# Kernel tuning notes

Hardware: AMD Instinct MI355X
Metric: run time of the kernel (lower is better)

The kernel has to match this reference:

```python
import jax, jax.numpy as jnp
import numpy as np

B_SZ, L_SEQ = 8, 2048
D_MODEL, N_STATE = 1024, 64
NUM_HEADS, N_REC = 1, 8
H_DIM = D_MODEL // NUM_HEADS


def setup_inputs() -> dict:
    key = jax.random.key(0)
    ks = jax.random.split(key, 12)
    Np = N_STATE
    return {
        "u": jax.random.normal(ks[0], (B_SZ, L_SEQ, D_MODEL), jnp.float32),
        "k_proj_w": jax.random.normal(ks[1], (D_MODEL, D_MODEL), jnp.float32) / np.float32(np.sqrt(D_MODEL)),
        "k_proj_b": jax.random.normal(ks[2], (D_MODEL,), jnp.float32) * 0.02,
        "shift_B": jax.random.normal(ks[3], (D_MODEL, Np), jnp.float32) / np.float32(np.sqrt(Np)),
        "shift_C": jax.random.normal(ks[4], (D_MODEL, Np), jnp.float32) / np.float32(np.sqrt(Np)),
        "ssm_k_D": jax.random.normal(ks[5], (D_MODEL,), jnp.float32),
        "log_dt": jax.random.uniform(ks[6], (H_DIM,), jnp.float32, minval=np.float32(np.log(1e-3)), maxval=np.float32(np.log(1e-1))),
        "log_A_real": jnp.log(0.5 * jnp.ones((H_DIM, Np), jnp.float32)),
        "A_imag": jnp.broadcast_to(np.float32(np.pi) * jnp.arange(Np, dtype=jnp.float32), (H_DIM, Np)),
        "B_re": jax.random.normal(ks[7], (H_DIM, Np), jnp.float32),
        "B_im": jax.random.normal(ks[8], (H_DIM, Np), jnp.float32),
    }


def _shift_kernel(Bp, Cp, L):
    # Shift-SSM kernel (SSKernel mode='shift'): K(l) = sum_m C[m+l] * B[m], zero for l >= N.
    N = Bp.shape[-1]
    nfft = 2 * N
    Bf = jnp.fft.rfft(Bp, n=nfft)
    Cf = jnp.fft.rfft(Cp, n=nfft)
    k = jnp.fft.irfft(Cf * jnp.conj(Bf), n=nfft)[..., :N]  # (D, N) linear cross-correlation
    return jnp.pad(k, ((0, 0), (0, L - N)))  # (D, L)


def _kernel_expand(k, log_dt, log_A_real, A_imag, B_re, B_im):
    # Diagonal-SSM state expansion: SSM states x_t = sum_{s<=t} dA^{t-s} dB u_s,
    # read out at N_REC evenly spaced chunk boundaries.
    # k: (B, G, H, L) real -> (B, N_REC, G, H, N) real
    Bb, G, H, L = k.shape
    Lc = L // N_REC
    dt = jnp.exp(log_dt)[:, None]                      # (H,1)
    A = -jnp.exp(log_A_real) + 1j * A_imag             # (H,N)
    dA_log = dt * A                                    # (H,N)
    dB = (B_re + 1j * B_im) * ((jnp.exp(dA_log) - 1.0) / A)  # ZOH discretization
    exps = jnp.arange(Lc - 1, -1, -1, dtype=jnp.float32)      # (Lc,)
    P = jnp.exp(dA_log[..., None] * exps) * dB[..., None]     # (H,N,Lc): dA^{Lc-1-i} dB
    kc = k.reshape(Bb, G, H, N_REC, Lc).astype(P.dtype)
    contrib = jnp.einsum('hnl,bghrl->rbghn', P, kc)           # (N_REC,B,G,H,N)
    dA_Lc = jnp.exp(dA_log * Lc)                              # (H,N)
    x0 = jnp.zeros((Bb, G, H, A.shape[-1]), P.dtype)

    def step(x, c):
        x = dA_Lc * x + c
        return x, x

    _, states = jax.lax.scan(step, x0, contrib)               # (N_REC,B,G,H,N)
    return jnp.transpose(states.real, (1, 0, 2, 3, 4))


def reference(u, k_proj_w, k_proj_b, shift_B, shift_C, ssm_k_D, log_dt, log_A_real, A_imag, B_re, B_im):
    Bb, L, D = u.shape
    # k = W @ u^T + b  -> (B, D, L)
    k = jnp.einsum('bld,hd->bhl', u, k_proj_w) + k_proj_b[None, :, None]
    Ks = _shift_kernel(shift_B, shift_C, L)  # (D, L)
    nfft = 2 * L  # fft_size = L_kernel + L
    conv = jnp.fft.irfft(jnp.fft.rfft(Ks, n=nfft)[None] * jnp.fft.rfft(k, n=nfft), n=nfft)[..., :L]
    k = conv + ssm_k_D[None, :, None] * k
    # rearrange 'b (h d1) l -> b d1 h l'
    k = k.reshape(Bb, H_DIM, NUM_HEADS, L).transpose(0, 2, 1, 3)
    return _kernel_expand(k, log_dt, log_A_real, A_imag, B_re, B_im)
```

## Files before the change

kernel.cpp:

```cpp
#include <hip/hip_runtime.h>
#include <cstddef>
#include <cstdint>

#define L_SEQ 2048
#define DM    1024
#define NREC  8
#define BM 128
#define BN 128
#define BK 32
#define NT (DM / BK)

typedef __attribute__((ext_vector_type(8))) short short8;
typedef __attribute__((ext_vector_type(4))) float f32x4;
typedef __attribute__((ext_vector_type(2))) unsigned int u32x2;

__device__ inline unsigned short f2bf(float f) {
    unsigned u = __float_as_uint(f);
    unsigned r = (u + 0x7FFFu + ((u >> 16) & 1u)) >> 16;
    return (unsigned short)r;
}
__device__ inline float bf2f(unsigned short s) {
    return __uint_as_float(((unsigned)s) << 16);
}
__device__ inline void gload_lds16(const void* g, void* l) {
    __builtin_amdgcn_global_load_lds(
        (const __attribute__((address_space(1))) void*)g,
        (__attribute__((address_space(3))) void*)l, 16, 0, 0);
}

__global__ __launch_bounds__(256) void cvt2_bf16(
    const float* __restrict__ a, unsigned short* __restrict__ oa, int na,
    const float* __restrict__ b, unsigned short* __restrict__ ob, int nb)
{
    int i = (blockIdx.x * 256 + threadIdx.x) * 8;
    const float* src;
    unsigned short* dst;
    if (i < na) { src = a + i; dst = oa + i; }
    else {
        int j = i - na;
        if (j >= nb) return;
        src = b + j; dst = ob + j;
    }
    f32x4 v0 = *(const f32x4*)(src);
    f32x4 v1 = *(const f32x4*)(src + 4);
    short8 o;
    o[0] = (short)f2bf(v0[0]); o[1] = (short)f2bf(v0[1]);
    o[2] = (short)f2bf(v0[2]); o[3] = (short)f2bf(v0[3]);
    o[4] = (short)f2bf(v1[0]); o[5] = (short)f2bf(v1[1]);
    o[6] = (short)f2bf(v1[2]); o[7] = (short)f2bf(v1[3]);
    *(short8*)dst = o;
}

template<bool PREW>
__global__ __launch_bounds__(256, 2) void gemm_klin(
    const float* __restrict__ Wf, const unsigned short* __restrict__ Wb,
    const unsigned short* __restrict__ ub,
    const float* __restrict__ bias, unsigned short* __restrict__ klin)
{
    __shared__ unsigned short As[2][BM * BK];
    __shared__ unsigned short Bs[2][BM * BK];
    int wg = (int)blockIdx.x;
    wg = (wg & 7) * 128 + (wg >> 3);
    const int b  = wg >> 7;
    const int h0 = ((wg >> 4) & 7) * BM;
    const int l0 = (wg & 15) * BN;
    const int tid = threadIdx.x;
    const int lane = tid & 63, wv = tid >> 6;

    const int r0 = wv * 32 + (lane >> 2);
    const int r1 = r0 + 16;
    const int sw0 = (r0 ^ (r0 >> 2)) & 3;
    const int sw1 = (r1 ^ (r1 >> 2)) & 3;
    const int col0 = (((lane & 3) ^ sw0) << 3);
    const int col1 = (((lane & 3) ^ sw1) << 3);

    const unsigned short* gB0 = ub + ((size_t)(b * L_SEQ + l0 + r0)) * DM + col0;
    const unsigned short* gB1 = ub + ((size_t)(b * L_SEQ + l0 + r1)) * DM + col1;
    const unsigned short* gA0b = Wb + (size_t)(h0 + r0) * DM + col0;
    const unsigned short* gA1b = Wb + (size_t)(h0 + r1) * DM + col1;
    const float* gA0f = Wf + (size_t)(h0 + r0) * DM + col0;
    const float* gA1f = Wf + (size_t)(h0 + r1) * DM + col1;

    const int wm = wv >> 1, wn = wv & 1;
    const int lr = lane & 15, lk = lane >> 4;

    f32x4 acc[4][4];
    #pragma unroll
    for (int m = 0; m < 4; ++m)
        #pragma unroll
        for (int n = 0; n < 4; ++n) acc[m][n] = (f32x4){0.f, 0.f, 0.f, 0.f};

    gload_lds16(gB0, &Bs[0][(2 * wv) * 512]);
    gload_lds16(gB1, &Bs[0][(2 * wv + 1) * 512]);
    if constexpr (PREW) {
        gload_lds16(gA0b, &As[0][(2 * wv) * 512]);
        gload_lds16(gA1b, &As[0][(2 * wv + 1) * 512]);
    } else {
        f32x4 a0 = *(const f32x4*)(gA0f);
        f32x4 a1 = *(const f32x4*)(gA0f + 4);
        f32x4 a2 = *(const f32x4*)(gA1f);
        f32x4 a3 = *(const f32x4*)(gA1f + 4);
        short8 c0, c1;
        c0[0]=(short)f2bf(a0[0]); c0[1]=(short)f2bf(a0[1]); c0[2]=(short)f2bf(a0[2]); c0[3]=(short)f2bf(a0[3]);
        c0[4]=(short)f2bf(a1[0]); c0[5]=(short)f2bf(a1[1]); c0[6]=(short)f2bf(a1[2]); c0[7]=(short)f2bf(a1[3]);
        c1[0]=(short)f2bf(a2[0]); c1[1]=(short)f2bf(a2[1]); c1[2]=(short)f2bf(a2[2]); c1[3]=(short)f2bf(a2[3]);
        c1[4]=(short)f2bf(a3[0]); c1[5]=(short)f2bf(a3[1]); c1[6]=(short)f2bf(a3[2]); c1[7]=(short)f2bf(a3[3]);
        *(short8*)&As[0][r0 * 32 + (lane & 3) * 8] = c0;
        *(short8*)&As[0][r1 * 32 + (lane & 3) * 8] = c1;
    }

    for (int kt = 0; kt < NT; ++kt) {
        __syncthreads();
        const int bf = kt & 1;
        const bool more = (kt + 1 < NT);
        f32x4 a0, a1, a2, a3;
        if (more) {
            const int ko = (kt + 1) * BK;
            gload_lds16(gB0 + ko, &Bs[bf ^ 1][(2 * wv) * 512]);
            gload_lds16(gB1 + ko, &Bs[bf ^ 1][(2 * wv + 1) * 512]);
            if constexpr (PREW) {
                gload_lds16(gA0b + ko, &As[bf ^ 1][(2 * wv) * 512]);
                gload_lds16(gA1b + ko, &As[bf ^ 1][(2 * wv + 1) * 512]);
            } else {
                a0 = *(const f32x4*)(gA0f + ko);
                a1 = *(const f32x4*)(gA0f + ko + 4);
                a2 = *(const f32x4*)(gA1f + ko);
                a3 = *(const f32x4*)(gA1f + ko + 4);
            }
        }
        short8 af[4], bfr[4];
        #pragma unroll
        for (int m = 0; m < 4; ++m) {
            int row = wm * 64 + m * 16 + lr;
            int phys = lk ^ ((row ^ (row >> 2)) & 3);
            af[m] = *(const short8*)&As[bf][row * 32 + phys * 8];
        }
        #pragma unroll
        for (int n = 0; n < 4; ++n) {
            int row = wn * 64 + n * 16 + lr;
            int phys = lk ^ ((row ^ (row >> 2)) & 3);
            bfr[n] = *(const short8*)&Bs[bf][row * 32 + phys * 8];
        }
        #pragma unroll
        for (int m = 0; m < 4; ++m)
            #pragma unroll
            for (int n = 0; n < 4; ++n)
                acc[m][n] = __builtin_amdgcn_mfma_f32_16x16x32_bf16(af[m], bfr[n], acc[m][n], 0, 0, 0);
        if constexpr (!PREW) {
            if (more) {
                short8 c0, c1;
                c0[0]=(short)f2bf(a0[0]); c0[1]=(short)f2bf(a0[1]); c0[2]=(short)f2bf(a0[2]); c0[3]=(short)f2bf(a0[3]);
                c0[4]=(short)f2bf(a1[0]); c0[5]=(short)f2bf(a1[1]); c0[6]=(short)f2bf(a1[2]); c0[7]=(short)f2bf(a1[3]);
                c1[0]=(short)f2bf(a2[0]); c1[1]=(short)f2bf(a2[1]); c1[2]=(short)f2bf(a2[2]); c1[3]=(short)f2bf(a2[3]);
                c1[4]=(short)f2bf(a3[0]); c1[5]=(short)f2bf(a3[1]); c1[6]=(short)f2bf(a3[2]); c1[7]=(short)f2bf(a3[3]);
                *(short8*)&As[bf ^ 1][r0 * 32 + (lane & 3) * 8] = c0;
                *(short8*)&As[bf ^ 1][r1 * 32 + (lane & 3) * 8] = c1;
            }
        }
    }

    #pragma unroll
    for (int m = 0; m < 4; ++m) {
        const int h = h0 + wm * 64 + m * 16 + lk * 4;
        #pragma unroll
        for (int n = 0; n < 4; ++n) {
            const int l = l0 + wn * 64 + n * 16 + lr;
            #pragma unroll
            for (int r = 0; r < 4; ++r) {
                float v = acc[m][n][r] + bias[h + r];
                klin[((size_t)b * DM + h + r) * L_SEQ + l] = f2bf(v);
            }
        }
    }
}

__device__ inline void get_disc(const float* __restrict__ log_dt,
                                const float* __restrict__ lar,
                                const float* __restrict__ aim, int h, int n,
                                float& Are, float& Aim, float& lre, float& lim)
{
    float dtv = expf(log_dt[h]);
    Are = -expf(lar[h * 64 + n]);
    Aim = aim[h * 64 + n];
    lre = dtv * Are;
    lim = dtv * Aim;
}

__global__ __launch_bounds__(256, 2) void expand(
    const unsigned short* __restrict__ klin,
    const float* __restrict__ shift_B, const float* __restrict__ shift_C,
    const float* __restrict__ ssm_k_D, const float* __restrict__ log_dt,
    const float* __restrict__ log_A_real, const float* __restrict__ A_imag,
    const float* __restrict__ B_re, const float* __restrict__ B_im,
    float* __restrict__ out)
{
    __shared__ __align__(16) char sm[80384];
    constexpr int OKL = 0;
    constexpr int OKK = 34816;
    constexpr int OAF = 67584;
    constexpr int OPR = 70912;
    constexpr int OPI = 75008;
    constexpr int OF  = 79104;
    constexpr int OBS = 79360;
    constexpr int OCS = 79616;
    constexpr int OW32 = 79872;

    const int h = blockIdx.x;
    const int t = threadIdx.x;
    const int lane = t & 63, wv = t >> 6;

    {
        int q = lane & 15;
        int b = 2 * wv + (q >> 3);
        if (lane < 16)
            *(f32x4*)&sm[OKL + b * 4352 + (q & 7) * 16] = (f32x4){0.f, 0.f, 0.f, 0.f};
        else if (lane < 32)
            *(f32x4*)&sm[OKL + b * 4352 + 4224 + (q & 7) * 16] = (f32x4){0.f, 0.f, 0.f, 0.f};
    }
    #pragma unroll
    for (int rr = 0; rr < 2; ++rr) {
        const int b = 2 * wv + rr;
        const char* krow = (const char*)(klin + ((size_t)b * DM + h) * L_SEQ);
        const int s = (2 * b + 1 + (lane >> 3)) & 7;
        const int srcoff = (lane >> 3) * 128 + ((lane ^ s) & 7) * 16;
        #pragma unroll
        for (int c = 0; c < 4; ++c)
            gload_lds16(krow + c * 1024 + srcoff, &sm[OKL + b * 4352 + 128 + c * 1024]);
    }
    if (t < 64) {
        ((float*)&sm[OBS])[t] = shift_B[h * 64 + t];
        ((float*)&sm[OCS])[t] = shift_C[h * 64 + t];
        float Are, Aim, lre, lim;
        get_disc(log_dt, log_A_real, A_imag, h, t, Are, Aim, lre, lim);
        float er = expf(32.f * lre);
        float sn, cs; sincosf(32.f * lim, &sn, &cs);
        ((float*)&sm[OW32])[t * 2]     = er * cs;
        ((float*)&sm[OW32])[t * 2 + 1] = er * sn;
    }
    {
        int n = t >> 2, s4 = t & 3;
        float Are, Aim, lre, lim;
        get_disc(log_dt, log_A_real, A_imag, h, n, Are, Aim, lre, lim);
        float erw = expf(lre), snw, csw;
        sincosf(lim, &snw, &csw);
        float wr = erw * csw, wi = erw * snw;
        float e0 = (float)(24 - 8 * s4);
        float mag = expf(e0 * lre);
        float sn0, cs0; sincosf(e0 * lim, &sn0, &cs0);
        float pr = mag * cs0, pi = mag * sn0;
        float vr[8], vi[8];
        vr[7] = pr; vi[7] = pi;
        #pragma unroll
        for (int k = 6; k >= 0; --k) {
            float nr = pr * wr - pi * wi;
            pi = fmaf(pr, wi, pi * wr);
            pr = nr;
            vr[k] = pr; vi[k] = pi;
        }
        short8 re8, im8;
        #pragma unroll
        for (int e = 0; e < 8; ++e) {
            re8[e] = (short)f2bf(vr[e]);
            im8[e] = (short)f2bf(vi[e]);
        }
        *(short8*)&sm[OPR + t * 16] = re8;
        *(short8*)&sm[OPI + t * 16] = im8;
    }
    __syncthreads();

    if (t < 64) {
        const float* Bp = (const float*)&sm[OBS];
        const float* Cp = (const float*)&sm[OCS];
        float f = (t == 0) ? ssm_k_D[h] : 0.f;
        for (int j = 0; j + t < 64; ++j) f = fmaf(Cp[j + t], Bp[j], f);
        ((float*)&sm[OF])[t] = f;
    }
    __syncthreads();

    {
        int i = t >> 4, ks = t & 15;
        if (ks < 12) {
            const float* Fp = (const float*)&sm[OF];
            short8 row;
            #pragma unroll
            for (int e = 0; e < 8; ++e) {
                int k = ks * 8 + e;
                int m = 64 + i - k;
                float v = (m >= 0 && m < 64) ? Fp[m] : 0.f;
                row[e] = (short)f2bf(v);
            }
            *(short8*)&sm[OAF + i * 208 + ks * 16] = row;
        }
    }
    __syncthreads();

    {
        short8 afr[3];
        #pragma unroll
        for (int ks = 0; ks < 3; ++ks)
            afr[ks] = *(const short8*)&sm[OAF + (lane & 15) * 208 + ks * 64 + (lane >> 4) * 16];
        #pragma unroll
        for (int rr = 0; rr < 2; ++rr) {
            const int b = 2 * wv + rr;
            #pragma unroll
            for (int jg = 0; jg < 8; ++jg) {
                f32x4 d = (f32x4){0.f, 0.f, 0.f, 0.f};
                #pragma unroll
                for (int ks = 0; ks < 3; ++ks) {
                    int o = b * 4352 + (jg * 256 + (lane & 15) * 16 + ks * 32 + (lane >> 4) * 8) * 2;
                    o ^= ((o >> 7) & 7) << 4;
                    short8 bfrag = *(const short8*)&sm[OKL + o];
                    d = __builtin_amdgcn_mfma_f32_16x16x32_bf16(afr[ks], bfrag, d, 0, 0, 0);
                }
                unsigned pk0 = ((unsigned)f2bf(d[0])) | (((unsigned)f2bf(d[1])) << 16);
                unsigned pk1 = ((unsigned)f2bf(d[2])) | (((unsigned)f2bf(d[3])) << 16);
                int o2 = b * 4096 + jg * 512 + (lane & 15) * 32 + (lane >> 4) * 8;
                o2 ^= ((o2 >> 9) & 7) << 4;
                *(u32x2*)&sm[OKK + o2] = (u32x2){pk0, pk1};
            }
        }
    }
    __syncthreads();

    {
        short8 par[4], pai[4];
        #pragma unroll
        for (int mt = 0; mt < 4; ++mt) {
            int o = (mt * 16 + (lane & 15)) * 64 + (lane >> 4) * 16;
            par[mt] = *(const short8*)&sm[OPR + o];
            pai[mt] = *(const short8*)&sm[OPI + o];
        }
        float w32r[16], w32i[16];
        #pragma unroll
        for (int mt = 0; mt < 4; ++mt)
            #pragma unroll
            for (int rg = 0; rg < 4; ++rg) {
                int n = mt * 16 + (lane >> 4) * 4 + rg;
                float2 ww = *(const float2*)&sm[OW32 + n * 8];
                w32r[mt * 4 + rg] = ww.x;
                w32i[mt * 4 + rg] = ww.y;
            }
        f32x4 cr[4], ci_[4];
        #pragma unroll
        for (int mt = 0; mt < 4; ++mt) {
            cr[mt] = (f32x4){0.f, 0.f, 0.f, 0.f};
            ci_[mt] = (f32x4){0.f, 0.f, 0.f, 0.f};
        }
        const int colb = 2 * wv + ((lane & 15) >> 3);
        const int colr = lane & 7;
        #pragma unroll
        for (int g = 0; g < 8; ++g) {
            int o = colb * 4096 + colr * 512 + g * 64 + (lane >> 4) * 16;
            o ^= ((o >> 9) & 7) << 4;
            short8 kf = *(const short8*)&sm[OKK + o];
            #pragma unroll
            for (int mt = 0; mt < 4; ++mt) {
                f32x4 sre = __builtin_amdgcn_mfma_f32_16x16x32_bf16(par[mt], kf, (f32x4){0.f,0.f,0.f,0.f}, 0, 0, 0);
                f32x4 sim = __builtin_amdgcn_mfma_f32_16x16x32_bf16(pai[mt], kf, (f32x4){0.f,0.f,0.f,0.f}, 0, 0, 0);
                #pragma unroll
                for (int rg = 0; rg < 4; ++rg) {
                    float wr = w32r[mt * 4 + rg], wi = w32i[mt * 4 + rg];
                    float ncr = fmaf(cr[mt][rg], wr, fmaf(-ci_[mt][rg], wi, sre[rg]));
                    float nci = fmaf(cr[mt][rg], wi, fmaf(ci_[mt][rg], wr, sim[rg]));
                    cr[mt][rg] = ncr;
                    ci_[mt][rg] = nci;
                }
            }
        }
        #pragma unroll
        for (int mt = 0; mt < 4; ++mt)
            #pragma unroll
            for (int rg = 0; rg < 4; ++rg) {
                int n = mt * 16 + (lane >> 4) * 4 + rg;
                int col = wv * 16 + (lane & 15);
                ((float*)&sm[OKL])[n * 68 + col] = cr[mt][rg];
                ((float*)&sm[OKL + 17408])[n * 68 + col] = ci_[mt][rg];
            }
    }
    __syncthreads();

    {
        const int n = t & 63;
        float Are, Aim, lre, lim;
        get_disc(log_dt, log_A_real, A_imag, h, n, Are, Aim, lre, lim);
        float er = expf(lre), sn, cs;
        sincosf(lim, &sn, &cs);
        float wr = er * cs, wi = er * sn;
        float2 w32v = *(const float2*)&sm[OW32 + n * 8];
        float ar = w32v.x, ai = w32v.y;
        #pragma unroll
        for (int s = 0; s < 3; ++s) {
            float nr = ar * ar - ai * ai;
            ai = 2.f * ar * ai;
            ar = nr;
        }
        float den = Are * Are + Aim * Aim;
        float wm1r = wr - 1.f, wm1i = wi;
        float tr_ = (wm1r * Are + wm1i * Aim) / den;
        float ti_ = (wm1i * Are - wm1r * Aim) / den;
        float br = B_re[h * 64 + n], bi = B_im[h * 64 + n];
        float dBr = br * tr_ - bi * ti_;
        float dBi = br * ti_ + bi * tr_;
        #pragma unroll
        for (int half = 0; half < 2; ++half) {
            int b = (t >> 6) + 4 * half;
            const float* cre = (const float*)&sm[OKL] + n * 68 + b * 8;
            const float* cim = (const float*)&sm[OKL + 17408] + n * 68 + b * 8;
            float sr = 0.f, si_ = 0.f;
            #pragma unroll
            for (int r = 0; r < 8; ++r) {
                float nsr = fmaf(ar, sr, fmaf(-ai, si_, cre[r]));
                float nsi = fmaf(ar, si_, fmaf(ai, sr, cim[r]));
                sr = nsr; si_ = nsi;
                out[(((size_t)b * NREC + r) * DM + h) * 64 + n] = dBr * sr - dBi * si_;
            }
        }
    }
}

extern "C" void kernel_launch(void* const* d_in, const int* in_sizes, int n_in,
                              void* d_out, int out_size, void* d_ws, size_t ws_size,
                              hipStream_t stream)
{
    const float* u       = (const float*)d_in[0];
    const float* W       = (const float*)d_in[1];
    const float* bias    = (const float*)d_in[2];
    const float* shift_B = (const float*)d_in[3];
    const float* shift_C = (const float*)d_in[4];
    const float* ssm_k_D = (const float*)d_in[5];
    const float* log_dt  = (const float*)d_in[6];
    const float* log_Ar  = (const float*)d_in[7];
    const float* A_imag  = (const float*)d_in[8];
    const float* B_re    = (const float*)d_in[9];
    const float* B_im    = (const float*)d_in[10];
    float* out = (float*)d_out;

    const int n_u = 8 * L_SEQ * DM;
    const int n_w = DM * DM;
    unsigned short* ub   = (unsigned short*)d_ws;
    unsigned short* klin = ub + (size_t)n_u;
    unsigned short* Wb   = klin + (size_t)n_u;

    const bool prew = ws_size >= (size_t)66 * 1024 * 1024;

    if (prew) {
        cvt2_bf16<<<(n_u + n_w) / (256 * 8), 256, 0, stream>>>(u, ub, n_u, W, Wb, n_w);
        gemm_klin<true><<<dim3(1024), 256, 0, stream>>>(W, Wb, ub, bias, klin);
    } else {
        cvt2_bf16<<<n_u / (256 * 8), 256, 0, stream>>>(u, ub, n_u, W, Wb, 0);
        gemm_klin<false><<<dim3(1024), 256, 0, stream>>>(W, Wb, ub, bias, klin);
    }

    expand<<<dim3(DM), 256, 0, stream>>>(klin, shift_B, shift_C, ssm_k_D, log_dt,
                                         log_Ar, A_imag, B_re, B_im, out);
}
```

Before: 90.63 us.

## Split expand kernel across batch groups to cut LDS and raise occupancy

The expand kernel now launches a 2D grid (channel × 4 batch groups), so each block handles 2 batches instead of 8. Its shared memory drops from about 80KB to about 29KB and launch bounds rise to 5 blocks per CU, which gives more parallelism and latency hiding. The cost is that per-channel setup (discretization, P matrices, Toeplitz filter) is recomputed in each of the four blocks, and only half the threads do the final scan. The shift-correlation loop is also made fixed-length with a mask so it can be unrolled.

```diff
diff --git a/kernel.cpp b/kernel.cpp
--- a/kernel.cpp
+++ b/kernel.cpp
@@ -186,7 +186,7 @@
     lim = dtv * Aim;
 }
 
-__global__ __launch_bounds__(256, 2) void expand(
+__global__ __launch_bounds__(256, 5) void expand(
     const unsigned short* __restrict__ klin,
     const float* __restrict__ shift_B, const float* __restrict__ shift_C,
     const float* __restrict__ ssm_k_D, const float* __restrict__ log_dt,
@@ -194,38 +194,34 @@
     const float* __restrict__ B_re, const float* __restrict__ B_im,
     float* __restrict__ out)
 {
-    __shared__ __align__(16) char sm[80384];
+    __shared__ __align__(16) char sm[29696];
     constexpr int OKL = 0;
-    constexpr int OKK = 34816;
-    constexpr int OAF = 67584;
-    constexpr int OPR = 70912;
-    constexpr int OPI = 75008;
-    constexpr int OF  = 79104;
-    constexpr int OBS = 79360;
-    constexpr int OCS = 79616;
-    constexpr int OW32 = 79872;
-
-    const int h = blockIdx.x;
+    constexpr int OKK = 8704;
+    constexpr int OAF = 16896;
+    constexpr int OPR = 20224;
+    constexpr int OPI = 24320;
+    constexpr int OF  = 28416;
+    constexpr int OBS = 28672;
+    constexpr int OCS = 28928;
+    constexpr int OW32 = 29184;
+
+    const int h  = blockIdx.x;
+    const int bg = blockIdx.y;
     const int t = threadIdx.x;
     const int lane = t & 63, wv = t >> 6;
 
+    if (t < 32) {
+        int rl = t >> 4, reg = (t >> 3) & 1, idx = t & 7;
+        *(f32x4*)&sm[OKL + rl * 4352 + reg * 4224 + idx * 16] = (f32x4){0.f, 0.f, 0.f, 0.f};
+    }
     {
-        int q = lane & 15;
-        int b = 2 * wv + (q >> 3);
-        if (lane < 16)
-            *(f32x4*)&sm[OKL + b * 4352 + (q & 7) * 16] = (f32x4){0.f, 0.f, 0.f, 0.f};
-        else if (lane < 32)
-            *(f32x4*)&sm[OKL + b * 4352 + 4224 + (q & 7) * 16] = (f32x4){0.f, 0.f, 0.f, 0.f};
-    }
-    #pragma unroll
-    for (int rr = 0; rr < 2; ++rr) {
-        const int b = 2 * wv + rr;
+        const int rl = wv >> 1, hf = wv & 1;
+        const int b = bg * 2 + rl;
         const char* krow = (const char*)(klin + ((size_t)b * DM + h) * L_SEQ);
-        const int s = (2 * b + 1 + (lane >> 3)) & 7;
-        const int srcoff = (lane >> 3) * 128 + ((lane ^ s) & 7) * 16;
-        #pragma unroll
-        for (int c = 0; c < 4; ++c)
-            gload_lds16(krow + c * 1024 + srcoff, &sm[OKL + b * 4352 + 128 + c * 1024]);
+        const int s = (2 * rl + 1 + (lane >> 3)) & 7;
+        const int so = hf * 2048 + (lane >> 3) * 128 + ((lane ^ s) & 7) * 16;
+        gload_lds16(krow + so,        &sm[OKL + rl * 4352 + 128 + hf * 2048]);
+        gload_lds16(krow + so + 1024, &sm[OKL + rl * 4352 + 128 + hf * 2048 + 1024]);
     }
     if (t < 64) {
         ((float*)&sm[OBS])[t] = shift_B[h * 64 + t];
@@ -272,7 +268,11 @@
         const float* Bp = (const float*)&sm[OBS];
         const float* Cp = (const float*)&sm[OCS];
         float f = (t == 0) ? ssm_k_D[h] : 0.f;
-        for (int j = 0; j + t < 64; ++j) f = fmaf(Cp[j + t], Bp[j], f);
+        #pragma unroll 8
+        for (int j = 0; j < 64; ++j) {
+            float cv = Cp[(j + t) & 63];
+            f = fmaf((j + t < 64) ? cv : 0.f, Bp[j], f);
+        }
         ((float*)&sm[OF])[t] = f;
     }
     __syncthreads();
@@ -299,88 +299,74 @@
         #pragma unroll
         for (int ks = 0; ks < 3; ++ks)
             afr[ks] = *(const short8*)&sm[OAF + (lane & 15) * 208 + ks * 64 + (lane >> 4) * 16];
-        #pragma unroll
-        for (int rr = 0; rr < 2; ++rr) {
-            const int b = 2 * wv + rr;
+        const int rl = wv >> 1;
+        const int jbase = (wv & 1) * 4;
+        #pragma unroll
+        for (int jj = 0; jj < 4; ++jj) {
+            const int jg = jbase + jj;
+            f32x4 d = (f32x4){0.f, 0.f, 0.f, 0.f};
             #pragma unroll
-            for (int jg = 0; jg < 8; ++jg) {
-                f32x4 d = (f32x4){0.f, 0.f, 0.f, 0.f};
-                #pragma unroll
-                for (int ks = 0; ks < 3; ++ks) {
-                    int o = b * 4352 + (jg * 256 + (lane & 15) * 16 + ks * 32 + (lane >> 4) * 8) * 2;
-                    o ^= ((o >> 7) & 7) << 4;
-                    short8 bfrag = *(const short8*)&sm[OKL + o];
-                    d = __builtin_amdgcn_mfma_f32_16x16x32_bf16(afr[ks], bfrag, d, 0, 0, 0);
-                }
-                unsigned pk0 = ((unsigned)f2bf(d[0])) | (((unsigned)f2bf(d[1])) << 16);
-                unsigned pk1 = ((unsigned)f2bf(d[2])) | (((unsigned)f2bf(d[3])) << 16);
-                int o2 = b * 4096 + jg * 512 + (lane & 15) * 32 + (lane >> 4) * 8;
-                o2 ^= ((o2 >> 9) & 7) << 4;
-                *(u32x2*)&sm[OKK + o2] = (u32x2){pk0, pk1};
-            }
+            for (int ks = 0; ks < 3; ++ks) {
+                int o = rl * 4352 + (jg * 256 + (lane & 15) * 16 + ks * 32 + (lane >> 4) * 8) * 2;
+                o ^= ((o >> 7) & 7) << 4;
+                short8 bfrag = *(const short8*)&sm[OKL + o];
+                d = __builtin_amdgcn_mfma_f32_16x16x32_bf16(afr[ks], bfrag, d, 0, 0, 0);
+            }
+            unsigned pk0 = ((unsigned)f2bf(d[0])) | (((unsigned)f2bf(d[1])) << 16);
+            unsigned pk1 = ((unsigned)f2bf(d[2])) | (((unsigned)f2bf(d[3])) << 16);
+            int o2 = rl * 4096 + jg * 512 + (lane & 15) * 32 + (lane >> 4) * 8;
+            o2 ^= ((o2 >> 9) & 7) << 4;
+            *(u32x2*)&sm[OKK + o2] = (u32x2){pk0, pk1};
         }
     }
     __syncthreads();
 
     {
-        short8 par[4], pai[4];
-        #pragma unroll
-        for (int mt = 0; mt < 4; ++mt) {
-            int o = (mt * 16 + (lane & 15)) * 64 + (lane >> 4) * 16;
-            par[mt] = *(const short8*)&sm[OPR + o];
-            pai[mt] = *(const short8*)&sm[OPI + o];
-        }
-        float w32r[16], w32i[16];
-        #pragma unroll
-        for (int mt = 0; mt < 4; ++mt)
-            #pragma unroll
-            for (int rg = 0; rg < 4; ++rg) {
-                int n = mt * 16 + (lane >> 4) * 4 + rg;
-                float2 ww = *(const float2*)&sm[OW32 + n * 8];
-                w32r[mt * 4 + rg] = ww.x;
-                w32i[mt * 4 + rg] = ww.y;
-            }
-        f32x4 cr[4], ci_[4];
-        #pragma unroll
-        for (int mt = 0; mt < 4; ++mt) {
-            cr[mt] = (f32x4){0.f, 0.f, 0.f, 0.f};
-            ci_[mt] = (f32x4){0.f, 0.f, 0.f, 0.f};
-        }
-        const int colb = 2 * wv + ((lane & 15) >> 3);
+        const int mt = wv;
+        short8 par = *(const short8*)&sm[OPR + (mt * 16 + (lane & 15)) * 64 + (lane >> 4) * 16];
+        short8 pai = *(const short8*)&sm[OPI + (mt * 16 + (lane & 15)) * 64 + (lane >> 4) * 16];
+        float w32r[4], w32i[4];
+        #pragma unroll
+        for (int rg = 0; rg < 4; ++rg) {
+            int n = mt * 16 + (lane >> 4) * 4 + rg;
+            float2 ww = *(const float2*)&sm[OW32 + n * 8];
+            w32r[rg] = ww.x;
+            w32i[rg] = ww.y;
+        }
+        f32x4 cr = (f32x4){0.f, 0.f, 0.f, 0.f};
+        f32x4 ci_ = (f32x4){0.f, 0.f, 0.f, 0.f};
+        const int colb = (lane & 15) >> 3;
         const int colr = lane & 7;
         #pragma unroll
         for (int g = 0; g < 8; ++g) {
             int o = colb * 4096 + colr * 512 + g * 64 + (lane >> 4) * 16;
             o ^= ((o >> 9) & 7) << 4;
             short8 kf = *(const short8*)&sm[OKK + o];
-            #pragma unroll
-            for (int mt = 0; mt < 4; ++mt) {
-                f32x4 sre = __builtin_amdgcn_mfma_f32_16x16x32_bf16(par[mt], kf, (f32x4){0.f,0.f,0.f,0.f}, 0, 0, 0);
-                f32x4 sim = __builtin_amdgcn_mfma_f32_16x16x32_bf16(pai[mt], kf, (f32x4){0.f,0.f,0.f,0.f}, 0, 0, 0);
-                #pragma unroll
-                for (int rg = 0; rg < 4; ++rg) {
-                    float wr = w32r[mt * 4 + rg], wi = w32i[mt * 4 + rg];
-                    float ncr = fmaf(cr[mt][rg], wr, fmaf(-ci_[mt][rg], wi, sre[rg]));
-                    float nci = fmaf(cr[mt][rg], wi, fmaf(ci_[mt][rg], wr, sim[rg]));
-                    cr[mt][rg] = ncr;
-                    ci_[mt][rg] = nci;
-                }
-            }
-        }
-        #pragma unroll
-        for (int mt = 0; mt < 4; ++mt)
+            f32x4 sre = __builtin_amdgcn_mfma_f32_16x16x32_bf16(par, kf, (f32x4){0.f,0.f,0.f,0.f}, 0, 0, 0);
+            f32x4 sim = __builtin_amdgcn_mfma_f32_16x16x32_bf16(pai, kf, (f32x4){0.f,0.f,0.f,0.f}, 0, 0, 0);
             #pragma unroll
             for (int rg = 0; rg < 4; ++rg) {
-                int n = mt * 16 + (lane >> 4) * 4 + rg;
-                int col = wv * 16 + (lane & 15);
-                ((float*)&sm[OKL])[n * 68 + col] = cr[mt][rg];
-                ((float*)&sm[OKL + 17408])[n * 68 + col] = ci_[mt][rg];
-            }
+                float wr = w32r[rg], wi = w32i[rg];
+                float ncr = fmaf(cr[rg], wr, fmaf(-ci_[rg], wi, sre[rg]));
+                float nci = fmaf(cr[rg], wi, fmaf(ci_[rg], wr, sim[rg]));
+                cr[rg] = ncr;
+                ci_[rg] = nci;
+            }
+        }
+        __syncthreads();
+        #pragma unroll
+        for (int rg = 0; rg < 4; ++rg) {
+            int n = mt * 16 + (lane >> 4) * 4 + rg;
+            int c = lane & 15;
+            ((float*)&sm[OKK])[n * 17 + c] = cr[rg];
+            ((float*)&sm[OKK])[1088 + n * 17 + c] = ci_[rg];
+        }
     }
     __syncthreads();
 
-    {
-        const int n = t & 63;
+    if (t < 128) {
+        const int n = t & 63, bl = t >> 6;
+        const int b = bg * 2 + bl;
         float Are, Aim, lre, lim;
         get_disc(log_dt, log_A_real, A_imag, h, n, Are, Aim, lre, lim);
         float er = expf(lre), sn, cs;
@@ -401,19 +387,15 @@
         float br = B_re[h * 64 + n], bi = B_im[h * 64 + n];
         float dBr = br * tr_ - bi * ti_;
         float dBi = br * ti_ + bi * tr_;
-        #pragma unroll
-        for (int half = 0; half < 2; ++half) {
-            int b = (t >> 6) + 4 * half;
-            const float* cre = (const float*)&sm[OKL] + n * 68 + b * 8;
-            const float* cim = (const float*)&sm[OKL + 17408] + n * 68 + b * 8;
-            float sr = 0.f, si_ = 0.f;
-            #pragma unroll
-            for (int r = 0; r < 8; ++r) {
-                float nsr = fmaf(ar, sr, fmaf(-ai, si_, cre[r]));
-                float nsi = fmaf(ar, si_, fmaf(ai, sr, cim[r]));
-                sr = nsr; si_ = nsi;
-                out[(((size_t)b * NREC + r) * DM + h) * 64 + n] = dBr * sr - dBi * si_;
-            }
+        const float* cre = (const float*)&sm[OKK] + n * 17 + bl * 8;
+        const float* cim = (const float*)&sm[OKK] + 1088 + n * 17 + bl * 8;
+        float sr = 0.f, si_ = 0.f;
+        #pragma unroll
+        for (int r = 0; r < 8; ++r) {
+            float nsr = fmaf(ar, sr, fmaf(-ai, si_, cre[r]));
+            float nsi = fmaf(ar, si_, fmaf(ai, sr, cim[r]));
+            sr = nsr; si_ = nsi;
+            out[(((size_t)b * NREC + r) * DM + h) * 64 + n] = dBr * sr - dBi * si_;
         }
     }
 }
@@ -451,6 +433,6 @@
         gemm_klin<false><<<dim3(1024), 256, 0, stream>>>(W, Wb, ub, bias, klin);
     }
 
-    expand<<<dim3(DM), 256, 0, stream>>>(klin, shift_B, shift_C, ssm_k_D, log_dt,
-                                         log_Ar, A_imag, B_re, B_im, out);
-}
+    expand<<<dim3(DM, 4), 256, 0, stream>>>(klin, shift_B, shift_C, ssm_k_D, log_dt,
+                                            log_Ar, A_imag, B_re, B_im, out);
+}
```

After: 88.19 us. 2.7% less time.
